# Kernel optimization log

Measured on AMD Instinct MI355X. Metric: run time of the kernel, lower is better.

The kernel has to match this reference:

```python
import jax, jax.numpy as jnp
import numpy as np

B, C, W, H = 4, 256, 64, 64
D = C // 8  # reduced query/key channels


def setup_inputs() -> dict:
    key = jax.random.key(0)
    k1, k2, k3, k4, k5 = jax.random.split(key, 5)
    return {
        "x": jax.random.normal(k1, (B, C, W, H), dtype=jnp.float32),
        "q_weight": jax.random.normal(k2, (D, C), dtype=jnp.float32) * 0.05,
        "k_weight": jax.random.normal(k3, (D, C), dtype=jnp.float32) * 0.05,
        "v_weight": jax.random.normal(k4, (C, C), dtype=jnp.float32) * 0.05,
        "gamma": jax.random.normal(k5, (1,), dtype=jnp.float32),
    }


def reference(x, q_weight, k_weight, v_weight, gamma):
    b, c, w, h = x.shape
    n = w * h
    xf = x.reshape(b, c, n)                       # (B, C, N)
    # 1x1 convs == channel matmuls
    q = jnp.einsum('dc,bcn->bdn', q_weight, xf)   # (B, D, N)
    k = jnp.einsum('dc,bcn->bdn', k_weight, xf)   # (B, D, N)
    v = jnp.einsum('oc,bcn->bon', v_weight, xf)   # (B, C, N)
    # energy[b, i, j] = <q[:, i], k[:, j]>  (unscaled, single head)
    energy = jnp.einsum('bdi,bdj->bij', q, k)     # (B, N, N)
    attn = jax.nn.softmax(energy, axis=-1)        # softmax over keys j
    # out[b, c, i] = sum_j v[b, c, j] * attn[b, i, j]
    out = jnp.einsum('bcj,bij->bci', v, attn)     # (B, C, N)
    out = out.reshape(b, c, w, h)
    return gamma[0] * out + x
```

## Files before the change

### kernel.cpp

```cpp
#include <hip/hip_runtime.h>
#include <math.h>

#define Bb 4
#define Cc 256
#define Nn 4096
#define Dd 32
#define XST 264

typedef __attribute__((ext_vector_type(8))) short bf16x8;
typedef __attribute__((ext_vector_type(4))) float f32x4;

__device__ __forceinline__ unsigned short f2bf(float x) {
    union { float f; unsigned u; } c; c.f = x;
    unsigned r = c.u + 0x7fffu + ((c.u >> 16) & 1u);
    return (unsigned short)(r >> 16);
}
__device__ __forceinline__ unsigned pk2(float a, float b) {
    return (unsigned)f2bf(a) | ((unsigned)f2bf(b) << 16);
}
__device__ __forceinline__ void load_lds16(const void* g, void* l) {
    __builtin_amdgcn_global_load_lds(
        (const __attribute__((address_space(1))) void*)g,
        (__attribute__((address_space(3))) void*)l, 16, 0, 0);
}
__device__ __forceinline__ float fexp2(float x) {
#if __has_builtin(__builtin_amdgcn_exp2f)
    return __builtin_amdgcn_exp2f(x);
#else
    return __exp2f(x);
#endif
}
template <int CTRL>
__device__ __forceinline__ float dppf(float v) {
    int iv = __builtin_bit_cast(int, v);
    return __builtin_bit_cast(float,
        __builtin_amdgcn_update_dpp(iv, iv, CTRL, 0xF, 0xF, false));
}
__device__ __forceinline__ float rowsum16(float v) {
    v += dppf<0xB1>(v);
    v += dppf<0x4E>(v);
    v += dppf<0x141>(v);
    v += dppf<0x140>(v);
    return v;
}

__global__ __launch_bounds__(256) void pack_w(
    const float* __restrict__ qw, const float* __restrict__ kw,
    const float* __restrict__ vw, short* __restrict__ wpk) {
    const int g = blockIdx.x * 256 + threadIdx.x;
    const int qd = g & 3, m = (g >> 2) & 15, kc = (g >> 6) & 7, ot = g >> 9;
    const int o = 16 * ot + m;
    const float* src;
    float scale = 1.0f;
    if (o < 32)      { src = qw + (size_t)o * Cc; scale = 1.44269504088896f; }
    else if (o < 64) { src = kw + (size_t)(o - 32) * Cc; }
    else             { src = vw + (size_t)(o - 64) * Cc; }
    const float* s8 = src + 32 * kc + 8 * qd;
    uint4 u;
    u.x = pk2(s8[0] * scale, s8[1] * scale);
    u.y = pk2(s8[2] * scale, s8[3] * scale);
    u.z = pk2(s8[4] * scale, s8[5] * scale);
    u.w = pk2(s8[6] * scale, s8[7] * scale);
    *(uint4*)(wpk + (size_t)g * 8) = u;
}

__global__ __launch_bounds__(256) void proj(
    const float* __restrict__ x, const short* __restrict__ wpk,
    short* __restrict__ q_t, short* __restrict__ k_t, short* __restrict__ v_b) {
    __shared__ alignas(16) short xs[32 * XST];
    const int b = blockIdx.z;
    const int n0 = blockIdx.x * 32;
    const int tid = threadIdx.x;
    const int w = tid >> 6;
    const int lane = tid & 63, qd = lane >> 4, m = lane & 15;

    {
        const int n = tid & 31, cg = tid >> 5;
        const float* xp = x + ((size_t)b * Cc + 32 * cg) * Nn + n0 + n;
        float xv[32];
#pragma unroll
        for (int i = 0; i < 32; ++i) xv[i] = xp[(size_t)i * Nn];
        short* row = xs + n * XST + 32 * cg;
#pragma unroll
        for (int u4 = 0; u4 < 4; ++u4)
            *(uint4*)(row + 8 * u4) = make_uint4(
                pk2(xv[8*u4+0], xv[8*u4+1]), pk2(xv[8*u4+2], xv[8*u4+3]),
                pk2(xv[8*u4+4], xv[8*u4+5]), pk2(xv[8*u4+6], xv[8*u4+7]));
    }
    __syncthreads();

    const int fslot = m * 4 + qd;
    f32x4 acc[5][2];
#pragma unroll
    for (int i = 0; i < 5; ++i)
#pragma unroll
        for (int nt = 0; nt < 2; ++nt) acc[i][nt] = (f32x4){0.f, 0.f, 0.f, 0.f};

    bf16x8 afc[5], afn[5];
#pragma unroll
    for (int i = 0; i < 5; ++i)
        afc[i] = *(const bf16x8*)(wpk + ((size_t)((4*i + w) * 8 + 0) * 64 + fslot) * 8);

    for (int kc = 0; kc < 8; ++kc) {
        if (kc < 7) {
#pragma unroll
            for (int i = 0; i < 5; ++i)
                afn[i] = *(const bf16x8*)(
                    wpk + ((size_t)((4*i + w) * 8 + kc + 1) * 64 + fslot) * 8);
        }
        const bf16x8 b0 = *(const bf16x8*)&xs[(     m) * XST + 32 * kc + 8 * qd];
        const bf16x8 b1 = *(const bf16x8*)&xs[(16 + m) * XST + 32 * kc + 8 * qd];
#pragma unroll
        for (int i = 0; i < 5; ++i)
            acc[i][0] = __builtin_amdgcn_mfma_f32_16x16x32_bf16(afc[i], b0, acc[i][0], 0, 0, 0);
#pragma unroll
        for (int i = 0; i < 5; ++i)
            acc[i][1] = __builtin_amdgcn_mfma_f32_16x16x32_bf16(afc[i], b1, acc[i][1], 0, 0, 0);
#pragma unroll
        for (int i = 0; i < 5; ++i) afc[i] = afn[i];
    }

#pragma unroll
    for (int i = 0; i < 5; ++i) {
        const int ot = 4 * i + w;
        if (ot < 4) {
            short* dst = (ot < 2 ? q_t : k_t) + (size_t)b * Nn * Dd;
            const int dbase = (ot & 1) * 16 + 4 * qd;
#pragma unroll
            for (int nt = 0; nt < 2; ++nt) {
                const f32x4 a = acc[i][nt];
                *(uint2*)(dst + (size_t)(n0 + 16 * nt + m) * Dd + dbase) =
                    make_uint2(pk2(a[0], a[1]), pk2(a[2], a[3]));
            }
        } else {
            const int ct = ot - 4;
            const int jt = n0 >> 6;
            const int b5 = (n0 >> 5) & 1;
            const size_t vbase =
                (((size_t)(b * 64 + jt) * 32 + ct * 2 + (m >> 3)) * 64
                 + ((m >> 1) & 3) * 16 + 4 * qd) * 8 + 4 * (m & 1) + 2 * b5;
#pragma unroll
            for (int rr = 0; rr < 4; ++rr) {
                const unsigned pv = pk2(acc[i][0][rr], acc[i][1][rr]);
                *(unsigned*)(v_b + vbase + rr * 8) = pv;
            }
        }
    }
}

__global__ __launch_bounds__(256) void attn(
    const float* __restrict__ x, const short* __restrict__ q_t,
    const short* __restrict__ k_t, const short* __restrict__ v_b,
    const float* __restrict__ gamma, float* __restrict__ out) {
    __shared__ alignas(16) char pool[17408];
    short* p_s = (short*)(pool + 8192);
    float* l_s = (float*)(pool + 16896);
    float* o_t = (float*)pool;

    const int fb  = blockIdx.x;
    const int xcd = fb & 7;
    const int b   = xcd >> 1;
    const int i0  = (((xcd & 1) << 6) | (fb >> 3)) << 5;
    const int tid = threadIdx.x;
    const int w = tid >> 6, lane = tid & 63;
    const int qd = lane >> 4, m = lane & 15;
    const int rt = w & 1, kh = w >> 1;

    const short* ktb = k_t + (size_t)b * Nn * Dd;

    const bf16x8 af = *(const bf16x8*)(
        q_t + ((size_t)b * Nn + i0 + 16 * rt + m) * Dd + 8 * qd);

    load_lds16(ktb + tid * 8, pool + tid * 16);

    f32x4 oacc[2][4];
#pragma unroll
    for (int mt = 0; mt < 2; ++mt)
#pragma unroll
        for (int ct = 0; ct < 4; ++ct) oacc[mt][ct] = (f32x4){0.f, 0.f, 0.f, 0.f};
    float l_i[4] = {0.f, 0.f, 0.f, 0.f};

    __syncthreads();

    int cur = 0;
    for (int jt = 0; jt < Nn / 64; ++jt) {
        const short* k_s = (const short*)(pool + 4096 * cur);
        if (jt) __syncthreads();

        bf16x8 vf[4][2];
#pragma unroll
        for (int ct = 0; ct < 4; ++ct)
#pragma unroll
            for (int kc = 0; kc < 2; ++kc)
                vf[ct][kc] = *(const bf16x8*)(
                    v_b + ((((size_t)(b * 64 + jt)) * 32 +
                            (4 * w + ct) * 2 + kc) * 64 + lane) * 8);

        const bf16x8 bk0 = *(const bf16x8*)(k_s + (16 * (2 * kh + 0) + m) * Dd + 8 * qd);
        const bf16x8 bk1 = *(const bf16x8*)(k_s + (16 * (2 * kh + 1) + m) * Dd + 8 * qd);
        const f32x4 s0 = __builtin_amdgcn_mfma_f32_16x16x32_bf16(
            af, bk0, (f32x4){0.f, 0.f, 0.f, 0.f}, 0, 0, 0);
        const f32x4 s1 = __builtin_amdgcn_mfma_f32_16x16x32_bf16(
            af, bk1, (f32x4){0.f, 0.f, 0.f, 0.f}, 0, 0, 0);

#pragma unroll
        for (int rr = 0; rr < 4; ++rr) {
            const float p0 = fexp2(s0[rr]);
            const float p1 = fexp2(s1[rr]);
            l_i[rr] += p0 + p1;
            *(unsigned*)&p_s[(16 * rt + 4 * qd + rr) * 72 + 4 * m + 2 * kh] =
                pk2(p0, p1);
        }
        __syncthreads();

        if (jt + 1 < Nn / 64)
            load_lds16(ktb + (size_t)(jt + 1) * 2048 + tid * 8,
                       pool + 4096 * (cur ^ 1) + tid * 16);

        __builtin_amdgcn_s_setprio(1);
#pragma unroll
        for (int kc = 0; kc < 2; ++kc) {
            bf16x8 pa[2];
#pragma unroll
            for (int mt = 0; mt < 2; ++mt)
                pa[mt] = *(const bf16x8*)&p_s[(16 * mt + m) * 72 + 32 * kc + 8 * qd];
#pragma unroll
            for (int ct = 0; ct < 4; ++ct)
#pragma unroll
                for (int mt = 0; mt < 2; ++mt)
                    oacc[mt][ct] = __builtin_amdgcn_mfma_f32_16x16x32_bf16(
                        pa[mt], vf[ct][kc], oacc[mt][ct], 0, 0, 0);
        }
        __builtin_amdgcn_s_setprio(0);
        cur ^= 1;
    }

#pragma unroll
    for (int rr = 0; rr < 4; ++rr) l_i[rr] = rowsum16(l_i[rr]);
    if (m == 0)
        *(f32x4*)&l_s[kh * 32 + 16 * rt + 4 * qd] =
            (f32x4){l_i[0], l_i[1], l_i[2], l_i[3]};
    __syncthreads();

    const float g = gamma[0];
    const int i = tid & 31, cg8 = tid >> 5;
    const float linv = 1.0f / (l_s[i] + l_s[32 + i]);
#pragma unroll
    for (int ps = 0; ps < 2; ++ps) {
        if (ps) __syncthreads();
#pragma unroll
        for (int ctp = 0; ctp < 2; ++ctp)
#pragma unroll
            for (int mt = 0; mt < 2; ++mt)
#pragma unroll
                for (int rr = 0; rr < 4; ++rr)
                    o_t[(16 * mt + 4 * qd + rr) * 132 + 32 * w + 16 * ctp + m] =
                        oacc[mt][2 * ps + ctp][rr];
        __syncthreads();
#pragma unroll
        for (int u = 0; u < 4; ++u) {
            const f32x4 v4 = *(const f32x4*)&o_t[i * 132 + 16 * cg8 + 4 * u];
#pragma unroll
            for (int e = 0; e < 4; ++e) {
                const int col = 16 * cg8 + 4 * u + e;
                const int c = 64 * (col >> 5) + 32 * ps + (col & 31);
                const size_t gidx = ((size_t)b * Cc + c) * Nn + i0 + i;
                out[gidx] = g * v4[e] * linv + x[gidx];
            }
        }
    }
}

extern "C" void kernel_launch(void* const* d_in, const int* in_sizes, int n_in,
                              void* d_out, int out_size, void* d_ws, size_t ws_size,
                              hipStream_t stream) {
    const float* x     = (const float*)d_in[0];
    const float* qw    = (const float*)d_in[1];
    const float* kw    = (const float*)d_in[2];
    const float* vw    = (const float*)d_in[3];
    const float* gamma = (const float*)d_in[4];
    float* out = (float*)d_out;

    short* q_t = (short*)d_ws;
    short* k_t = q_t + (size_t)Bb * Nn * Dd;
    short* v_b = k_t + (size_t)Bb * Nn * Dd;
    short* wpk = v_b + (size_t)Bb * Cc * Nn;

    pack_w<<<dim3(40), 256, 0, stream>>>(qw, kw, vw, wpk);
    proj<<<dim3(Nn / 32, 1, Bb), 256, 0, stream>>>(x, wpk, q_t, k_t, v_b);
    attn<<<dim3(512), 256, 0, stream>>>(x, q_t, k_t, v_b, gamma, out);
}
```

Before: 150.1 us.

## Replace LDS K staging with register double-buffered K/V prefetch in attention loop

Drops the global-to-LDS async copy of the K tile. Each wave now loads its K fragments and V fragments straight into registers, double-buffered (A/B) and prefetched one tile ahead, with the loop unrolled by two and the P buffer alternating between two LDS regions. This cuts one barrier per iteration and hides global load latency behind the MFMA work. It also sets launch_bounds min-blocks to 2, which raises register pressure and risks spills or lower occupancy.

```diff
diff --git a/kernel.cpp b/kernel.cpp
--- a/kernel.cpp
+++ b/kernel.cpp
@@ -17,11 +17,6 @@
 }
 __device__ __forceinline__ unsigned pk2(float a, float b) {
     return (unsigned)f2bf(a) | ((unsigned)f2bf(b) << 16);
-}
-__device__ __forceinline__ void load_lds16(const void* g, void* l) {
-    __builtin_amdgcn_global_load_lds(
-        (const __attribute__((address_space(1))) void*)g,
-        (__attribute__((address_space(3))) void*)l, 16, 0, 0);
 }
 __device__ __forceinline__ float fexp2(float x) {
 #if __has_builtin(__builtin_amdgcn_exp2f)
@@ -148,12 +143,11 @@
     }
 }
 
-__global__ __launch_bounds__(256) void attn(
+__global__ __launch_bounds__(256, 2) void attn(
     const float* __restrict__ x, const short* __restrict__ q_t,
     const short* __restrict__ k_t, const short* __restrict__ v_b,
     const float* __restrict__ gamma, float* __restrict__ out) {
     __shared__ alignas(16) char pool[17408];
-    short* p_s = (short*)(pool + 8192);
     float* l_s = (float*)(pool + 16896);
     float* o_t = (float*)pool;
 
@@ -166,12 +160,22 @@
     const int qd = lane >> 4, m = lane & 15;
     const int rt = w & 1, kh = w >> 1;
 
-    const short* ktb = k_t + (size_t)b * Nn * Dd;
-
     const bf16x8 af = *(const bf16x8*)(
         q_t + ((size_t)b * Nn + i0 + 16 * rt + m) * Dd + 8 * qd);
 
-    load_lds16(ktb + tid * 8, pool + tid * 16);
+    const short* kf = k_t + (size_t)b * Nn * Dd + (32 * kh + m) * Dd + 8 * qd;
+    const short* vw = v_b + (size_t)b * (64 * 32 * 64 * 8) + w * 4096 + lane * 8;
+
+    bf16x8 bkA0 = *(const bf16x8*)(kf);
+    bf16x8 bkA1 = *(const bf16x8*)(kf + 512);
+    bf16x8 bkB0 = *(const bf16x8*)(kf + 2048);
+    bf16x8 bkB1 = *(const bf16x8*)(kf + 2560);
+    bf16x8 vfA[4][2], vfB[4][2];
+#pragma unroll
+    for (int ct = 0; ct < 4; ++ct)
+#pragma unroll
+        for (int kc = 0; kc < 2; ++kc)
+            vfA[ct][kc] = *(const bf16x8*)(vw + (2 * ct + kc) * 512);
 
     f32x4 oacc[2][4];
 #pragma unroll
@@ -180,59 +184,95 @@
         for (int ct = 0; ct < 4; ++ct) oacc[mt][ct] = (f32x4){0.f, 0.f, 0.f, 0.f};
     float l_i[4] = {0.f, 0.f, 0.f, 0.f};
 
-    __syncthreads();
-
-    int cur = 0;
-    for (int jt = 0; jt < Nn / 64; ++jt) {
-        const short* k_s = (const short*)(pool + 4096 * cur);
-        if (jt) __syncthreads();
-
-        bf16x8 vf[4][2];
-#pragma unroll
-        for (int ct = 0; ct < 4; ++ct)
-#pragma unroll
-            for (int kc = 0; kc < 2; ++kc)
-                vf[ct][kc] = *(const bf16x8*)(
-                    v_b + ((((size_t)(b * 64 + jt)) * 32 +
-                            (4 * w + ct) * 2 + kc) * 64 + lane) * 8);
-
-        const bf16x8 bk0 = *(const bf16x8*)(k_s + (16 * (2 * kh + 0) + m) * Dd + 8 * qd);
-        const bf16x8 bk1 = *(const bf16x8*)(k_s + (16 * (2 * kh + 1) + m) * Dd + 8 * qd);
-        const f32x4 s0 = __builtin_amdgcn_mfma_f32_16x16x32_bf16(
-            af, bk0, (f32x4){0.f, 0.f, 0.f, 0.f}, 0, 0, 0);
-        const f32x4 s1 = __builtin_amdgcn_mfma_f32_16x16x32_bf16(
-            af, bk1, (f32x4){0.f, 0.f, 0.f, 0.f}, 0, 0, 0);
-
-#pragma unroll
-        for (int rr = 0; rr < 4; ++rr) {
-            const float p0 = fexp2(s0[rr]);
-            const float p1 = fexp2(s1[rr]);
-            l_i[rr] += p0 + p1;
-            *(unsigned*)&p_s[(16 * rt + 4 * qd + rr) * 72 + 4 * m + 2 * kh] =
-                pk2(p0, p1);
-        }
-        __syncthreads();
-
-        if (jt + 1 < Nn / 64)
-            load_lds16(ktb + (size_t)(jt + 1) * 2048 + tid * 8,
-                       pool + 4096 * (cur ^ 1) + tid * 16);
-
-        __builtin_amdgcn_s_setprio(1);
-#pragma unroll
-        for (int kc = 0; kc < 2; ++kc) {
-            bf16x8 pa[2];
-#pragma unroll
-            for (int mt = 0; mt < 2; ++mt)
-                pa[mt] = *(const bf16x8*)&p_s[(16 * mt + m) * 72 + 32 * kc + 8 * qd];
+    const short* kpre = kf + 4096;
+    const short* vpre = vw + 16384;
+
+    for (int j2 = 0; j2 < 32; ++j2) {
+        const bool pre = (j2 < 31);
+        {
+            short* ps = (short*)pool;
+            const f32x4 s0 = __builtin_amdgcn_mfma_f32_16x16x32_bf16(
+                af, bkA0, (f32x4){0.f, 0.f, 0.f, 0.f}, 0, 0, 0);
+            const f32x4 s1 = __builtin_amdgcn_mfma_f32_16x16x32_bf16(
+                af, bkA1, (f32x4){0.f, 0.f, 0.f, 0.f}, 0, 0, 0);
+            if (pre) {
+                bkA0 = *(const bf16x8*)(kpre);
+                bkA1 = *(const bf16x8*)(kpre + 512);
+            }
+#pragma unroll
+            for (int rr = 0; rr < 4; ++rr) {
+                const float p0 = fexp2(s0[rr]);
+                const float p1 = fexp2(s1[rr]);
+                l_i[rr] += p0 + p1;
+                *(unsigned*)&ps[(16 * rt + 4 * qd + rr) * 72 + 4 * m + 2 * kh] =
+                    pk2(p0, p1);
+            }
+            __syncthreads();
 #pragma unroll
             for (int ct = 0; ct < 4; ++ct)
 #pragma unroll
+                for (int kc = 0; kc < 2; ++kc)
+                    vfB[ct][kc] = *(const bf16x8*)(vpre + (2 * ct + kc) * 512);
+            __builtin_amdgcn_s_setprio(1);
+#pragma unroll
+            for (int kc = 0; kc < 2; ++kc) {
+                bf16x8 pa[2];
+#pragma unroll
                 for (int mt = 0; mt < 2; ++mt)
-                    oacc[mt][ct] = __builtin_amdgcn_mfma_f32_16x16x32_bf16(
-                        pa[mt], vf[ct][kc], oacc[mt][ct], 0, 0, 0);
-        }
-        __builtin_amdgcn_s_setprio(0);
-        cur ^= 1;
+                    pa[mt] = *(const bf16x8*)&ps[(16 * mt + m) * 72 + 32 * kc + 8 * qd];
+#pragma unroll
+                for (int ct = 0; ct < 4; ++ct)
+#pragma unroll
+                    for (int mt = 0; mt < 2; ++mt)
+                        oacc[mt][ct] = __builtin_amdgcn_mfma_f32_16x16x32_bf16(
+                            pa[mt], vfA[ct][kc], oacc[mt][ct], 0, 0, 0);
+            }
+            __builtin_amdgcn_s_setprio(0);
+        }
+        {
+            short* ps = (short*)(pool + 4608);
+            const f32x4 s0 = __builtin_amdgcn_mfma_f32_16x16x32_bf16(
+                af, bkB0, (f32x4){0.f, 0.f, 0.f, 0.f}, 0, 0, 0);
+            const f32x4 s1 = __builtin_amdgcn_mfma_f32_16x16x32_bf16(
+                af, bkB1, (f32x4){0.f, 0.f, 0.f, 0.f}, 0, 0, 0);
+            if (pre) {
+                bkB0 = *(const bf16x8*)(kpre + 2048);
+                bkB1 = *(const bf16x8*)(kpre + 2560);
+            }
+#pragma unroll
+            for (int rr = 0; rr < 4; ++rr) {
+                const float p0 = fexp2(s0[rr]);
+                const float p1 = fexp2(s1[rr]);
+                l_i[rr] += p0 + p1;
+                *(unsigned*)&ps[(16 * rt + 4 * qd + rr) * 72 + 4 * m + 2 * kh] =
+                    pk2(p0, p1);
+            }
+            __syncthreads();
+            if (pre) {
+#pragma unroll
+                for (int ct = 0; ct < 4; ++ct)
+#pragma unroll
+                    for (int kc = 0; kc < 2; ++kc)
+                        vfA[ct][kc] = *(const bf16x8*)(vpre + 16384 + (2 * ct + kc) * 512);
+            }
+            __builtin_amdgcn_s_setprio(1);
+#pragma unroll
+            for (int kc = 0; kc < 2; ++kc) {
+                bf16x8 pa[2];
+#pragma unroll
+                for (int mt = 0; mt < 2; ++mt)
+                    pa[mt] = *(const bf16x8*)&ps[(16 * mt + m) * 72 + 32 * kc + 8 * qd];
+#pragma unroll
+                for (int ct = 0; ct < 4; ++ct)
+#pragma unroll
+                    for (int mt = 0; mt < 2; ++mt)
+                        oacc[mt][ct] = __builtin_amdgcn_mfma_f32_16x16x32_bf16(
+                            pa[mt], vfB[ct][kc], oacc[mt][ct], 0, 0, 0);
+            }
+            __builtin_amdgcn_s_setprio(0);
+        }
+        kpre += 4096;
+        vpre += 32768;
     }
 
 #pragma unroll
```

Result: faster. 142.5 us (-5.0%).
